# Optimization experiments

Hardware: AMD Instinct MI355X
Metric: run time of the kernel (lower is better)

The kernel has to match this reference:

```python
import jax, jax.numpy as jnp
import numpy as np

H = 1024      # hidden_size
NH = 8        # num_attention_heads
HD = H // NH  # head dim = 128
FF = 3072     # DebertaConfig default intermediate_size
MAXPOS = 512  # max_position_embeddings
EPS = 1e-7    # DeBERTa layer_norm_eps


def layer_norm(x, g, b):
    m = jnp.mean(x, axis=-1, keepdims=True)
    v = jnp.mean((x - m) ** 2, axis=-1, keepdims=True)
    return (x - m) * jax.lax.rsqrt(v + EPS) * g + b


def setup_inputs() -> dict:
    key = jax.random.key(0)
    ks = jax.random.split(key, 12)
    s = 0.02  # init std
    B, S = 16, 512
    return {
        "x": jax.random.normal(ks[0], (B, S, H), jnp.float32),
        "pos_emb": jax.random.normal(ks[1], (MAXPOS, H), jnp.float32) * s,
        "emb_ln_g": jnp.ones((H,), jnp.float32),
        "emb_ln_b": jnp.zeros((H,), jnp.float32),
        "Wq": jax.random.normal(ks[2], (H, H), jnp.float32) * s,
        "Wk": jax.random.normal(ks[3], (H, H), jnp.float32) * s,
        "Wv": jax.random.normal(ks[4], (H, H), jnp.float32) * s,
        "q_bias": jax.random.normal(ks[5], (H,), jnp.float32) * s,
        "v_bias": jax.random.normal(ks[6], (H,), jnp.float32) * s,
        "Wo": jax.random.normal(ks[7], (H, H), jnp.float32) * s,
        "bo": jnp.zeros((H,), jnp.float32),
        "ln1_g": jnp.ones((H,), jnp.float32),
        "ln1_b": jnp.zeros((H,), jnp.float32),
        "Wi": jax.random.normal(ks[8], (H, FF), jnp.float32) * s,
        "bi": jnp.zeros((FF,), jnp.float32),
        "Wf": jax.random.normal(ks[9], (FF, H), jnp.float32) * s,
        "bf": jnp.zeros((H,), jnp.float32),
        "ln2_g": jnp.ones((H,), jnp.float32),
        "ln2_b": jnp.zeros((H,), jnp.float32),
    }


def reference(x, pos_emb, emb_ln_g, emb_ln_b, Wq, Wk, Wv, q_bias, v_bias,
              Wo, bo, ln1_g, ln1_b, Wi, bi, Wf, bf, ln2_g, ln2_b):
    B, S, _ = x.shape
    # DebertaEmbeddings: inputs_embeds + absolute position embeddings, LayerNorm (eval: no dropout)
    h = layer_norm(x + pos_emb[:S], emb_ln_g, emb_ln_b)
    # DisentangledSelfAttention with pos_att_type=[] -> standard attention, scale_factor=1;
    # in_proj has no bias, but q and v get learned bias vectors.
    q = (h @ Wq + q_bias).reshape(B, S, NH, HD).transpose(0, 2, 1, 3)  # [B,NH,S,HD]
    k = (h @ Wk).reshape(B, S, NH, HD).transpose(0, 2, 1, 3)
    v = (h @ Wv + v_bias).reshape(B, S, NH, HD).transpose(0, 2, 1, 3)
    scale = jnp.sqrt(jnp.asarray(HD, x.dtype))
    scores = jnp.einsum('bhqd,bhkd->bhqk', q / scale, k)  # [B,NH,S,S]
    probs = jax.nn.softmax(scores, axis=-1)  # attention_mask all ones -> plain softmax
    ctx = jnp.einsum('bhqk,bhkd->bhqd', probs, v)
    ctx = ctx.transpose(0, 2, 1, 3).reshape(B, S, H)
    # SelfOutput: dense + residual + LayerNorm
    attn_out = layer_norm(ctx @ Wo + bo + h, ln1_g, ln1_b)
    # Intermediate (exact gelu) + Output: dense + residual + LayerNorm
    ff = jax.nn.gelu(attn_out @ Wi + bi, approximate=False)
    out = layer_norm(ff @ Wf + bf + attn_out, ln2_g, ln2_b)
    return out
```

## Files before the change

### kernel.cpp

```cpp
#include <hip/hip_runtime.h>
#include <hip/hip_bf16.h>

#define BB  16
#define SS  512
#define HH  1024
#define NHH 8
#define HDD 128
#define FFF 3072
#define TT  (BB * SS)

typedef __hip_bfloat16 bf16;
typedef short s8v __attribute__((ext_vector_type(8)));
typedef float f4v __attribute__((ext_vector_type(4)));

__device__ __forceinline__ float bf2f(bf16 v) { return __bfloat162float(v); }
__device__ __forceinline__ bf16 f2bf(float f) { return __float2bfloat16(f); }
__device__ __forceinline__ float us2f(unsigned short u) {
  union { unsigned int i; float f; } c; c.i = (unsigned int)u << 16; return c.f;
}

__global__ void embed_ln_kernel(const float* __restrict__ x, const float* __restrict__ pos,
                                const float* __restrict__ g, const float* __restrict__ bta,
                                bf16* __restrict__ h) {
  int t = blockIdx.x;
  int s = t & (SS - 1);
  int tid = threadIdx.x;
  const float* xr = x + (size_t)t * HH;
  const float* pr = pos + (size_t)s * HH;
  float vals[4];
  float sum = 0.f;
#pragma unroll
  for (int i = 0; i < 4; i++) {
    int c = tid + i * 256;
    vals[i] = xr[c] + pr[c];
    sum += vals[i];
  }
  __shared__ float red[4];
#pragma unroll
  for (int off = 32; off > 0; off >>= 1) sum += __shfl_down(sum, off, 64);
  if ((tid & 63) == 0) red[tid >> 6] = sum;
  __syncthreads();
  float mean = (red[0] + red[1] + red[2] + red[3]) * (1.f / HH);
  float vsum = 0.f;
#pragma unroll
  for (int i = 0; i < 4; i++) { float d = vals[i] - mean; vsum += d * d; }
  __syncthreads();
#pragma unroll
  for (int off = 32; off > 0; off >>= 1) vsum += __shfl_down(vsum, off, 64);
  if ((tid & 63) == 0) red[tid >> 6] = vsum;
  __syncthreads();
  float rstd = rsqrtf((red[0] + red[1] + red[2] + red[3]) * (1.f / HH) + 1e-7f);
  bf16* hr = h + (size_t)t * HH;
#pragma unroll
  for (int i = 0; i < 4; i++) {
    int c = tid + i * 256;
    hr[c] = f2bf((vals[i] - mean) * rstd * g[c] + bta[c]);
  }
}

template <int OUT_F32>
__global__ void add_ln_kernel(const bf16* __restrict__ a, const bf16* __restrict__ res,
                              const float* __restrict__ g, const float* __restrict__ bta,
                              void* __restrict__ outv) {
  int t = blockIdx.x;
  int tid = threadIdx.x;
  const bf16* ar = a + (size_t)t * HH;
  const bf16* rr = res + (size_t)t * HH;
  float vals[4];
  float sum = 0.f;
#pragma unroll
  for (int i = 0; i < 4; i++) {
    int c = tid + i * 256;
    vals[i] = bf2f(ar[c]) + bf2f(rr[c]);
    sum += vals[i];
  }
  __shared__ float red[4];
#pragma unroll
  for (int off = 32; off > 0; off >>= 1) sum += __shfl_down(sum, off, 64);
  if ((tid & 63) == 0) red[tid >> 6] = sum;
  __syncthreads();
  float mean = (red[0] + red[1] + red[2] + red[3]) * (1.f / HH);
  float vsum = 0.f;
#pragma unroll
  for (int i = 0; i < 4; i++) { float d = vals[i] - mean; vsum += d * d; }
  __syncthreads();
#pragma unroll
  for (int off = 32; off > 0; off >>= 1) vsum += __shfl_down(vsum, off, 64);
  if ((tid & 63) == 0) red[tid >> 6] = vsum;
  __syncthreads();
  float rstd = rsqrtf((red[0] + red[1] + red[2] + red[3]) * (1.f / HH) + 1e-7f);
#pragma unroll
  for (int i = 0; i < 4; i++) {
    int c = tid + i * 256;
    float o = (vals[i] - mean) * rstd * g[c] + bta[c];
    if (OUT_F32)
      ((float*)outv)[(size_t)t * HH + c] = o;
    else
      ((bf16*)outv)[(size_t)t * HH + c] = f2bf(o);
  }
}

__global__ void convert_w_kernel(const float* __restrict__ W, bf16* __restrict__ Wt,
                                 int K, int N) {
  __shared__ float tile[32][33];
  int n0 = blockIdx.x * 32, k0 = blockIdx.y * 32;
#pragma unroll
  for (int it = 0; it < 4; it++) {
    int idx = threadIdx.x + it * 256;
    int ty = idx >> 5, tx = idx & 31;
    tile[ty][tx] = W[(size_t)(k0 + ty) * N + n0 + tx];
  }
  __syncthreads();
#pragma unroll
  for (int it = 0; it < 4; it++) {
    int idx = threadIdx.x + it * 256;
    int ty = idx >> 5, tx = idx & 31;
    Wt[(size_t)(n0 + ty) * K + k0 + tx] = f2bf(tile[tx][ty]);
  }
}

__global__ void transpose_v_kernel(const bf16* __restrict__ v, bf16* __restrict__ vt) {
  __shared__ unsigned short tile[32][33];
  int bh = blockIdx.z;
  int s0 = blockIdx.x * 32, d0 = blockIdx.y * 32;
  int b = bh >> 3, hd = bh & 7;
  const unsigned short* vp = (const unsigned short*)v + ((size_t)b * SS) * HH + hd * HDD;
  unsigned short* vtp = (unsigned short*)vt + (size_t)bh * HDD * SS;
#pragma unroll
  for (int it = 0; it < 4; it++) {
    int idx = threadIdx.x + it * 256;
    int ty = idx >> 5, tx = idx & 31;
    tile[ty][tx] = vp[(size_t)(s0 + ty) * HH + d0 + tx];
  }
  __syncthreads();
#pragma unroll
  for (int it = 0; it < 4; it++) {
    int idx = threadIdx.x + it * 256;
    int ty = idx >> 5, tx = idx & 31;
    vtp[(size_t)(d0 + ty) * SS + s0 + tx] = tile[tx][ty];
  }
}

template <int GELU>
__global__ __launch_bounds__(256)
void mfma_gemm_kernel(const bf16* __restrict__ A, int lda, long long sAb, long long sAh,
                      const bf16* __restrict__ Bt, int ldb, long long sBb, long long sBh,
                      const float* __restrict__ bias,
                      bf16* __restrict__ C, int ldc, long long sCb, long long sCh,
                      int M, int N, int K, float scale) {
  __shared__ unsigned short Als[128 * 40];
  __shared__ unsigned short Bls[128 * 40];
  int tid = threadIdx.x;
  int lane = tid & 63, wave = tid >> 6;
  int l15 = lane & 15, quad = lane >> 4;
  int wm = wave & 1, wn = wave >> 1;
  int m0 = blockIdx.y * 128, n0 = blockIdx.x * 128;
  int zb = blockIdx.z >> 3, zh = blockIdx.z & 7;
  const bf16* Ab = A + zb * sAb + zh * sAh;
  const bf16* Bb = Bt + zb * sBb + zh * sBh;
  bf16* Cb = C + zb * sCb + zh * sCh;
  f4v acc[4][4];
#pragma unroll
  for (int i = 0; i < 4; i++)
#pragma unroll
    for (int j = 0; j < 4; j++) acc[i][j] = (f4v){0.f, 0.f, 0.f, 0.f};
  int r0 = tid >> 2;
  int q8 = (tid & 3) * 8;
  for (int k0 = 0; k0 < K; k0 += 32) {
    uint4 a0 = *(const uint4*)(Ab + (size_t)(m0 + r0) * lda + k0 + q8);
    uint4 a1 = *(const uint4*)(Ab + (size_t)(m0 + r0 + 64) * lda + k0 + q8);
    uint4 b0 = *(const uint4*)(Bb + (size_t)(n0 + r0) * ldb + k0 + q8);
    uint4 b1 = *(const uint4*)(Bb + (size_t)(n0 + r0 + 64) * ldb + k0 + q8);
    *(uint4*)&Als[r0 * 40 + q8] = a0;
    *(uint4*)&Als[(r0 + 64) * 40 + q8] = a1;
    *(uint4*)&Bls[r0 * 40 + q8] = b0;
    *(uint4*)&Bls[(r0 + 64) * 40 + q8] = b1;
    __syncthreads();
    s8v af[4], bfr[4];
#pragma unroll
    for (int i = 0; i < 4; i++)
      af[i] = *(const s8v*)&Als[(wm * 64 + i * 16 + l15) * 40 + quad * 8];
#pragma unroll
    for (int j = 0; j < 4; j++)
      bfr[j] = *(const s8v*)&Bls[(wn * 64 + j * 16 + l15) * 40 + quad * 8];
#pragma unroll
    for (int i = 0; i < 4; i++)
#pragma unroll
      for (int j = 0; j < 4; j++)
        acc[i][j] = __builtin_amdgcn_mfma_f32_16x16x32_bf16(af[i], bfr[j], acc[i][j], 0, 0, 0);
    __syncthreads();
  }
#pragma unroll
  for (int i = 0; i < 4; i++) {
#pragma unroll
    for (int j = 0; j < 4; j++) {
      int n = n0 + wn * 64 + j * 16 + l15;
      float bval = bias ? bias[n] : 0.f;
#pragma unroll
      for (int r = 0; r < 4; r++) {
        int m = m0 + wm * 64 + i * 16 + quad * 4 + r;
        float v = (acc[i][j][r] + bval) * scale;
        if (GELU) v = 0.5f * v * (1.f + erff(v * 0.70710678118654752f));
        Cb[(size_t)m * ldc + n] = f2bf(v);
      }
    }
  }
}

__global__ void softmax_kernel(bf16* __restrict__ sc) {
  int wave = threadIdx.x >> 6, lane = threadIdx.x & 63;
  size_t row = (size_t)blockIdx.x * 4 + wave;
  unsigned short* p = (unsigned short*)sc + row * SS + lane * 8;
  union { uint4 u4; unsigned short u[8]; } buf;
  buf.u4 = *(const uint4*)p;
  float v[8];
  float mx = -1e30f;
#pragma unroll
  for (int j = 0; j < 8; j++) { v[j] = us2f(buf.u[j]); mx = fmaxf(mx, v[j]); }
#pragma unroll
  for (int off = 32; off > 0; off >>= 1) mx = fmaxf(mx, __shfl_xor(mx, off));
  float sum = 0.f;
#pragma unroll
  for (int j = 0; j < 8; j++) { v[j] = __expf(v[j] - mx); sum += v[j]; }
#pragma unroll
  for (int off = 32; off > 0; off >>= 1) sum += __shfl_xor(sum, off);
  float inv = 1.f / sum;
  union { uint4 u4; unsigned short u[8]; } obuf;
#pragma unroll
  for (int j = 0; j < 8; j++) {
    bf16 b = f2bf(v[j] * inv);
    obuf.u[j] = *(unsigned short*)&b;
  }
  *(uint4*)p = obuf.u4;
}

extern "C" void kernel_launch(void* const* d_in, const int* in_sizes, int n_in,
                              void* d_out, int out_size, void* d_ws, size_t ws_size,
                              hipStream_t stream) {
  const float* x     = (const float*)d_in[0];
  const float* pos   = (const float*)d_in[1];
  const float* eg    = (const float*)d_in[2];
  const float* ebeta = (const float*)d_in[3];
  const float* Wq    = (const float*)d_in[4];
  const float* Wk    = (const float*)d_in[5];
  const float* Wv    = (const float*)d_in[6];
  const float* qbias = (const float*)d_in[7];
  const float* vbias = (const float*)d_in[8];
  const float* Wo    = (const float*)d_in[9];
  const float* bo    = (const float*)d_in[10];
  const float* l1g   = (const float*)d_in[11];
  const float* l1b   = (const float*)d_in[12];
  const float* Wi    = (const float*)d_in[13];
  const float* bi    = (const float*)d_in[14];
  const float* Wf    = (const float*)d_in[15];
  const float* bfb   = (const float*)d_in[16];
  const float* l2g   = (const float*)d_in[17];
  const float* l2b   = (const float*)d_in[18];

  char* w = (char*)d_ws;
  const size_t MB = (size_t)1 << 20;
  bf16* h      = (bf16*)(w + 0 * MB);
  bf16* q      = (bf16*)(w + 16 * MB);
  bf16* k      = (bf16*)(w + 32 * MB);
  bf16* v      = (bf16*)(w + 48 * MB);
  bf16* ctx    = (bf16*)(w + 64 * MB);
  bf16* tmp1   = (bf16*)(w + 80 * MB);
  bf16* attn   = (bf16*)(w + 96 * MB);
  bf16* scores = (bf16*)(w + 112 * MB);
  bf16* ff     = (bf16*)(w + 112 * MB);
  bf16* tmp2   = (bf16*)(w + 176 * MB);
  bf16* vt     = (bf16*)(w + 192 * MB);
  bf16* Wqt    = (bf16*)(w + 208 * MB);
  bf16* Wkt    = (bf16*)(w + 210 * MB);
  bf16* Wvt    = (bf16*)(w + 212 * MB);
  bf16* Wot    = (bf16*)(w + 214 * MB);
  bf16* Wit    = (bf16*)(w + 216 * MB);
  bf16* Wft    = (bf16*)(w + 222 * MB);
  float* out   = (float*)d_out;

  const float QSCALE = 0.08838834764831845f;

  embed_ln_kernel<<<TT, 256, 0, stream>>>(x, pos, eg, ebeta, h);

  convert_w_kernel<<<dim3(HH / 32, HH / 32), 256, 0, stream>>>(Wq, Wqt, HH, HH);
  convert_w_kernel<<<dim3(HH / 32, HH / 32), 256, 0, stream>>>(Wk, Wkt, HH, HH);
  convert_w_kernel<<<dim3(HH / 32, HH / 32), 256, 0, stream>>>(Wv, Wvt, HH, HH);
  convert_w_kernel<<<dim3(HH / 32, HH / 32), 256, 0, stream>>>(Wo, Wot, HH, HH);
  convert_w_kernel<<<dim3(FFF / 32, HH / 32), 256, 0, stream>>>(Wi, Wit, HH, FFF);
  convert_w_kernel<<<dim3(HH / 32, FFF / 32), 256, 0, stream>>>(Wf, Wft, FFF, HH);

  mfma_gemm_kernel<0><<<dim3(8, 64, 1), 256, 0, stream>>>(
      h, HH, 0, 0, Wqt, HH, 0, 0, qbias, q, HH, 0, 0, TT, HH, HH, QSCALE);
  mfma_gemm_kernel<0><<<dim3(8, 64, 1), 256, 0, stream>>>(
      h, HH, 0, 0, Wkt, HH, 0, 0, nullptr, k, HH, 0, 0, TT, HH, HH, 1.f);
  mfma_gemm_kernel<0><<<dim3(8, 64, 1), 256, 0, stream>>>(
      h, HH, 0, 0, Wvt, HH, 0, 0, vbias, v, HH, 0, 0, TT, HH, HH, 1.f);

  mfma_gemm_kernel<0><<<dim3(4, 4, BB * NHH), 256, 0, stream>>>(
      q, HH, (long long)SS * HH, HDD,
      k, HH, (long long)SS * HH, HDD,
      nullptr,
      scores, SS, (long long)NHH * SS * SS, (long long)SS * SS,
      SS, SS, HDD, 1.f);

  softmax_kernel<<<BB * NHH * SS / 4, 256, 0, stream>>>(scores);

  transpose_v_kernel<<<dim3(SS / 32, HDD / 32, BB * NHH), 256, 0, stream>>>(v, vt);

  mfma_gemm_kernel<0><<<dim3(1, 4, BB * NHH), 256, 0, stream>>>(
      scores, SS, (long long)NHH * SS * SS, (long long)SS * SS,
      vt, SS, (long long)NHH * HDD * SS, (long long)HDD * SS,
      nullptr,
      ctx, HH, (long long)SS * HH, HDD,
      SS, HDD, SS, 1.f);

  mfma_gemm_kernel<0><<<dim3(8, 64, 1), 256, 0, stream>>>(
      ctx, HH, 0, 0, Wot, HH, 0, 0, bo, tmp1, HH, 0, 0, TT, HH, HH, 1.f);
  add_ln_kernel<0><<<TT, 256, 0, stream>>>(tmp1, h, l1g, l1b, attn);

  mfma_gemm_kernel<1><<<dim3(24, 64, 1), 256, 0, stream>>>(
      attn, HH, 0, 0, Wit, HH, 0, 0, bi, ff, FFF, 0, 0, TT, FFF, HH, 1.f);
  mfma_gemm_kernel<0><<<dim3(8, 64, 1), 256, 0, stream>>>(
      ff, FFF, 0, 0, Wft, FFF, 0, 0, bfb, tmp2, HH, 0, 0, TT, HH, FFF, 1.f);
  add_ln_kernel<1><<<TT, 256, 0, stream>>>(tmp2, attn, l2g, l2b, out);
}
```

Before: 611.9 us.

## Fuse Q/K/V projections into one GEMM and prefetch next K-tile in registers

Concatenates the transposed Wq/Wk/Wv weights into one buffer and runs a single 3H-wide projection GEMM with a combined bias vector (q bias, zeros, v bias). The attention-score GEMM and V transpose now read from the interleaved qkv buffer with a 3H stride, and the 1/sqrt(d) scale moves from the Q projection into the score GEMM. The GEMM main loop also register-prefetches the next K tile's global loads while the current tile is in LDS. The intent is to cut launch overhead and improve occupancy for the projections and to hide global load latency in every GEMM. The trade-offs are a strided qkv layout and extra live registers.

```diff
diff --git a/kernel.cpp b/kernel.cpp
--- a/kernel.cpp
+++ b/kernel.cpp
@@ -119,18 +119,28 @@
   }
 }
 
+__global__ void build_qkv_bias_kernel(const float* __restrict__ qb,
+                                      const float* __restrict__ vb,
+                                      float* __restrict__ o) {
+  int i = blockIdx.x * 256 + threadIdx.x;
+  float v = 0.f;
+  if (i < HH) v = qb[i];
+  else if (i >= 2 * HH) v = vb[i - 2 * HH];
+  o[i] = v;
+}
+
 __global__ void transpose_v_kernel(const bf16* __restrict__ v, bf16* __restrict__ vt) {
   __shared__ unsigned short tile[32][33];
   int bh = blockIdx.z;
   int s0 = blockIdx.x * 32, d0 = blockIdx.y * 32;
   int b = bh >> 3, hd = bh & 7;
-  const unsigned short* vp = (const unsigned short*)v + ((size_t)b * SS) * HH + hd * HDD;
+  const unsigned short* vp = (const unsigned short*)v + ((size_t)b * SS) * (3 * HH) + hd * HDD;
   unsigned short* vtp = (unsigned short*)vt + (size_t)bh * HDD * SS;
 #pragma unroll
   for (int it = 0; it < 4; it++) {
     int idx = threadIdx.x + it * 256;
     int ty = idx >> 5, tx = idx & 31;
-    tile[ty][tx] = vp[(size_t)(s0 + ty) * HH + d0 + tx];
+    tile[ty][tx] = vp[(size_t)(s0 + ty) * (3 * HH) + d0 + tx];
   }
   __syncthreads();
 #pragma unroll
@@ -166,16 +176,27 @@
     for (int j = 0; j < 4; j++) acc[i][j] = (f4v){0.f, 0.f, 0.f, 0.f};
   int r0 = tid >> 2;
   int q8 = (tid & 3) * 8;
+  const bf16* Ap0 = Ab + (size_t)(m0 + r0) * lda + q8;
+  const bf16* Ap1 = Ab + (size_t)(m0 + r0 + 64) * lda + q8;
+  const bf16* Bp0 = Bb + (size_t)(n0 + r0) * ldb + q8;
+  const bf16* Bp1 = Bb + (size_t)(n0 + r0 + 64) * ldb + q8;
+  uint4 a0 = *(const uint4*)(Ap0);
+  uint4 a1 = *(const uint4*)(Ap1);
+  uint4 b0 = *(const uint4*)(Bp0);
+  uint4 b1 = *(const uint4*)(Bp1);
   for (int k0 = 0; k0 < K; k0 += 32) {
-    uint4 a0 = *(const uint4*)(Ab + (size_t)(m0 + r0) * lda + k0 + q8);
-    uint4 a1 = *(const uint4*)(Ab + (size_t)(m0 + r0 + 64) * lda + k0 + q8);
-    uint4 b0 = *(const uint4*)(Bb + (size_t)(n0 + r0) * ldb + k0 + q8);
-    uint4 b1 = *(const uint4*)(Bb + (size_t)(n0 + r0 + 64) * ldb + k0 + q8);
     *(uint4*)&Als[r0 * 40 + q8] = a0;
     *(uint4*)&Als[(r0 + 64) * 40 + q8] = a1;
     *(uint4*)&Bls[r0 * 40 + q8] = b0;
     *(uint4*)&Bls[(r0 + 64) * 40 + q8] = b1;
     __syncthreads();
+    int kn = k0 + 32;
+    if (kn < K) {
+      a0 = *(const uint4*)(Ap0 + kn);
+      a1 = *(const uint4*)(Ap1 + kn);
+      b0 = *(const uint4*)(Bp0 + kn);
+      b1 = *(const uint4*)(Bp1 + kn);
+    }
     s8v af[4], bfr[4];
 #pragma unroll
     for (int i = 0; i < 4; i++)
@@ -260,9 +281,7 @@
   char* w = (char*)d_ws;
   const size_t MB = (size_t)1 << 20;
   bf16* h      = (bf16*)(w + 0 * MB);
-  bf16* q      = (bf16*)(w + 16 * MB);
-  bf16* k      = (bf16*)(w + 32 * MB);
-  bf16* v      = (bf16*)(w + 48 * MB);
+  bf16* qkv    = (bf16*)(w + 16 * MB);
   bf16* ctx    = (bf16*)(w + 64 * MB);
   bf16* tmp1   = (bf16*)(w + 80 * MB);
   bf16* attn   = (bf16*)(w + 96 * MB);
@@ -270,42 +289,38 @@
   bf16* ff     = (bf16*)(w + 112 * MB);
   bf16* tmp2   = (bf16*)(w + 176 * MB);
   bf16* vt     = (bf16*)(w + 192 * MB);
-  bf16* Wqt    = (bf16*)(w + 208 * MB);
-  bf16* Wkt    = (bf16*)(w + 210 * MB);
-  bf16* Wvt    = (bf16*)(w + 212 * MB);
+  bf16* Wqkvt  = (bf16*)(w + 208 * MB);
   bf16* Wot    = (bf16*)(w + 214 * MB);
   bf16* Wit    = (bf16*)(w + 216 * MB);
   bf16* Wft    = (bf16*)(w + 222 * MB);
+  float* qkvb  = (float*)(w + 228 * MB);
   float* out   = (float*)d_out;
 
   const float QSCALE = 0.08838834764831845f;
 
   embed_ln_kernel<<<TT, 256, 0, stream>>>(x, pos, eg, ebeta, h);
 
-  convert_w_kernel<<<dim3(HH / 32, HH / 32), 256, 0, stream>>>(Wq, Wqt, HH, HH);
-  convert_w_kernel<<<dim3(HH / 32, HH / 32), 256, 0, stream>>>(Wk, Wkt, HH, HH);
-  convert_w_kernel<<<dim3(HH / 32, HH / 32), 256, 0, stream>>>(Wv, Wvt, HH, HH);
+  convert_w_kernel<<<dim3(HH / 32, HH / 32), 256, 0, stream>>>(Wq, Wqkvt, HH, HH);
+  convert_w_kernel<<<dim3(HH / 32, HH / 32), 256, 0, stream>>>(Wk, Wqkvt + (size_t)HH * HH, HH, HH);
+  convert_w_kernel<<<dim3(HH / 32, HH / 32), 256, 0, stream>>>(Wv, Wqkvt + (size_t)2 * HH * HH, HH, HH);
   convert_w_kernel<<<dim3(HH / 32, HH / 32), 256, 0, stream>>>(Wo, Wot, HH, HH);
   convert_w_kernel<<<dim3(FFF / 32, HH / 32), 256, 0, stream>>>(Wi, Wit, HH, FFF);
   convert_w_kernel<<<dim3(HH / 32, FFF / 32), 256, 0, stream>>>(Wf, Wft, FFF, HH);
-
-  mfma_gemm_kernel<0><<<dim3(8, 64, 1), 256, 0, stream>>>(
-      h, HH, 0, 0, Wqt, HH, 0, 0, qbias, q, HH, 0, 0, TT, HH, HH, QSCALE);
-  mfma_gemm_kernel<0><<<dim3(8, 64, 1), 256, 0, stream>>>(
-      h, HH, 0, 0, Wkt, HH, 0, 0, nullptr, k, HH, 0, 0, TT, HH, HH, 1.f);
-  mfma_gemm_kernel<0><<<dim3(8, 64, 1), 256, 0, stream>>>(
-      h, HH, 0, 0, Wvt, HH, 0, 0, vbias, v, HH, 0, 0, TT, HH, HH, 1.f);
+  build_qkv_bias_kernel<<<12, 256, 0, stream>>>(qbias, vbias, qkvb);
+
+  mfma_gemm_kernel<0><<<dim3(24, 64, 1), 256, 0, stream>>>(
+      h, HH, 0, 0, Wqkvt, HH, 0, 0, qkvb, qkv, 3 * HH, 0, 0, TT, 3 * HH, HH, 1.f);
 
   mfma_gemm_kernel<0><<<dim3(4, 4, BB * NHH), 256, 0, stream>>>(
-      q, HH, (long long)SS * HH, HDD,
-      k, HH, (long long)SS * HH, HDD,
+      qkv, 3 * HH, (long long)SS * 3 * HH, HDD,
+      qkv + HH, 3 * HH, (long long)SS * 3 * HH, HDD,
       nullptr,
       scores, SS, (long long)NHH * SS * SS, (long long)SS * SS,
-      SS, SS, HDD, 1.f);
+      SS, SS, HDD, QSCALE);
 
   softmax_kernel<<<BB * NHH * SS / 4, 256, 0, stream>>>(scores);
 
-  transpose_v_kernel<<<dim3(SS / 32, HDD / 32, BB * NHH), 256, 0, stream>>>(v, vt);
+  transpose_v_kernel<<<dim3(SS / 32, HDD / 32, BB * NHH), 256, 0, stream>>>(qkv + 2 * HH, vt);
 
   mfma_gemm_kernel<0><<<dim3(1, 4, BB * NHH), 256, 0, stream>>>(
       scores, SS, (long long)NHH * SS * SS, (long long)SS * SS,
```

Measured after the change: 537.6 us. 12.1% less time.
